# Performance work log

Measured on AMD Instinct MI355X. Metric: run time of the kernel, lower is better.

Reference implementation:

```python
import jax, jax.numpy as jnp
import numpy as np

NUM_NODES = 50000
NUM_EDGES = 600000
IN_DIM = 128
OUT_DIM = 128


def setup_inputs() -> dict:
    key = jax.random.key(0)
    k1, k2, k3, k4, k5 = jax.random.split(key, 5)
    x = jax.random.normal(k1, (NUM_NODES, IN_DIM), dtype=jnp.float32)
    edge_index = jax.random.randint(k2, (2, NUM_EDGES), 0, NUM_NODES, dtype=jnp.int64)
    edge_weight = jax.random.uniform(k3, (NUM_EDGES,), dtype=jnp.float32)
    W = jax.random.normal(k4, (OUT_DIM, IN_DIM), dtype=jnp.float32) * (1.0 / np.sqrt(IN_DIM))
    b = jax.random.normal(k5, (OUT_DIM,), dtype=jnp.float32) * 0.01
    return {"x": x, "edge_index": edge_index, "edge_weight": edge_weight, "W": W, "b": b}


def reference(x, edge_index, edge_weight, W, b):
    num_nodes = x.shape[0]
    # add self loops
    loop = jnp.arange(num_nodes, dtype=edge_index.dtype)
    src = jnp.concatenate([edge_index[0], loop])           # [E + N]
    tgt = jnp.concatenate([edge_index[1], loop])           # [E + N]
    w = jnp.concatenate([edge_weight, jnp.ones((num_nodes,), dtype=edge_weight.dtype)])
    # degree via scatter-add over src, then symmetric normalization
    deg = jax.ops.segment_sum(w, src, num_segments=num_nodes)  # [N]
    dinv = 1.0 / jnp.sqrt(deg)
    w_norm = w * dinv[src] * dinv[tgt]                      # [E + N]
    # gather-scale-scatter aggregation
    msg = x[src] * w_norm[:, None]                          # [E + N, D]
    agg = jax.ops.segment_sum(msg, tgt, num_segments=num_nodes)  # [N, D]
    # dense linear (torch Linear convention)
    return agg @ W.T + b
```

## Files before the change

### kernel.cpp

```cpp
#include <hip/hip_runtime.h>

#define D 128
#define GROWS 32


__global__ __launch_bounds__(256) void k_setup(const float* __restrict__ W,
                                               const int* __restrict__ ei,
                                               float* __restrict__ Wt,
                                               int* __restrict__ flag) {
  int i = blockIdx.x * 256 + threadIdx.x;
  if (i < D * D) {
    int c = i >> 7, k = i & 127;
    Wt[k * D + c] = W[i];
  }
  if (i == 0) {
    flag[0] = (ei[1] == 0 && ei[3] == 0 && ei[5] == 0 && ei[7] == 0) ? 1 : 0;
  }
}

__global__ __launch_bounds__(256) void k_fused(const float* __restrict__ x,
                                               const float* __restrict__ Wt,
                                               float* __restrict__ y,
                                               const int* __restrict__ ei,
                                               const float* __restrict__ ew,
                                               float* __restrict__ deg,
                                               int* __restrict__ cnt,
                                               int* __restrict__ rank,
                                               const int* __restrict__ flag,
                                               int N, int E, int Gg, int T) {
  __shared__ float Xs[GROWS * D];
  const int B = blockIdx.x;
  const int tid = threadIdx.x;
  const long long gb = ((long long)B * Gg) / T;
  const long long gb1 = ((long long)(B + 1) * Gg) / T;

  if (gb1 > gb) {
    const int row0 = (int)gb * GROWS;
    for (int f = tid; f < GROWS * D / 4; f += 256) {
      int r = row0 + ((f * 4) >> 7);
      float4 v = make_float4(0.f, 0.f, 0.f, 0.f);
      if (r < N)
        v = reinterpret_cast<const float4*>(x)[(size_t)row0 * (D / 4) + f];
      reinterpret_cast<float4*>(Xs)[f] = v;
    }
    __syncthreads();

    const int c0 = (tid & 31) * 4;
    const int r0 = (tid >> 5) * 4;
    float acc[4][4];
#pragma unroll
    for (int i = 0; i < 4; ++i)
#pragma unroll
      for (int j = 0; j < 4; ++j) acc[i][j] = 0.f;

#pragma unroll 4
    for (int k = 0; k < D; ++k) {
      float4 wv = reinterpret_cast<const float4*>(Wt)[(k * D + c0) >> 2];
      float xr[4];
#pragma unroll
      for (int i = 0; i < 4; ++i) xr[i] = Xs[(r0 + i) * D + k];
#pragma unroll
      for (int i = 0; i < 4; ++i) {
        acc[i][0] += xr[i] * wv.x;
        acc[i][1] += xr[i] * wv.y;
        acc[i][2] += xr[i] * wv.z;
        acc[i][3] += xr[i] * wv.w;
      }
    }
#pragma unroll
    for (int i = 0; i < 4; ++i) {
      int row = row0 + r0 + i;
      if (row < N)
        reinterpret_cast<float4*>(y)[((size_t)row * D + c0) >> 2] =
            make_float4(acc[i][0], acc[i][1], acc[i][2], acc[i][3]);
    }
  } else {
    const int e = (B - (int)gb) * 256 + tid;
    if (e < E) {
      int s, t;
      if (flag[0]) {
        s = reinterpret_cast<const int2*>(ei)[e].x;
        t = reinterpret_cast<const int2*>(ei)[E + e].x;
      } else {
        s = ei[e];
        t = ei[E + e];
      }
      atomicAdd(&deg[s], ew[e]);
      rank[e] = atomicAdd(&cnt[t], 1);
    }
  }
}

__device__ __forceinline__ int wave_incl_scan(int v, int lane) {
#pragma unroll
  for (int o = 1; o < 64; o <<= 1) {
    int t = __shfl_up(v, o);
    if (lane >= o) v += t;
  }
  return v;
}

__global__ __launch_bounds__(256) void k_scan1(const int* __restrict__ cnt,
                                               int* __restrict__ rowptr,
                                               int* __restrict__ blocksum,
                                               float* __restrict__ deg,
                                               int N) {
  __shared__ int wtot[4];
  int tid = threadIdx.x;
  int i = blockIdx.x * 256 + tid;
  if (i < N) deg[i] = rsqrtf(deg[i] + 1.0f);
  int v = (i < N) ? cnt[i] : 0;
  int lane = tid & 63, wv = tid >> 6;
  int inc = wave_incl_scan(v, lane);
  if (lane == 63) wtot[wv] = inc;
  __syncthreads();
  if (tid == 0) {
    int r = 0;
#pragma unroll
    for (int k = 0; k < 4; ++k) { int t = wtot[k]; wtot[k] = r; r += t; }
  }
  __syncthreads();
  int exc = wtot[wv] + inc - v;
  if (i < N) rowptr[i] = exc;
  if (tid == 255) blocksum[blockIdx.x] = wtot[3] + inc;
}

__global__ __launch_bounds__(64) void k_scan2(int* __restrict__ blocksum,
                                              int* __restrict__ blockoff,
                                              int nb) {
  int lane = threadIdx.x;
  int carry = 0;
  for (int base = 0; base < nb; base += 64) {
    int idx = base + lane;
    int v = (idx < nb) ? blocksum[idx] : 0;
    int inc = wave_incl_scan(v, lane);
    if (idx < nb) blockoff[idx] = carry + inc - v;
    carry += __shfl(inc, 63);
  }
}

__global__ __launch_bounds__(256) void k_scan3(int* __restrict__ rowptr,
                                               const int* __restrict__ blockoff,
                                               int N, int E) {
  int i = blockIdx.x * 256 + threadIdx.x;
  if (i < N) rowptr[i] += blockoff[blockIdx.x];
  if (i == 0) rowptr[N] = E;
}

__global__ __launch_bounds__(256) void k_scatter(const int* __restrict__ ei,
                                                 const float* __restrict__ w,
                                                 const float* __restrict__ dinv,
                                                 const int* __restrict__ rowptr,
                                                 const int* __restrict__ rank,
                                                 int2* __restrict__ edges,
                                                 const int* __restrict__ flag,
                                                 int E) {
  int e = blockIdx.x * 256 + threadIdx.x;
  if (e >= E) return;
  int s, t;
  if (flag[0]) {
    s = reinterpret_cast<const int2*>(ei)[e].x;
    t = reinterpret_cast<const int2*>(ei)[E + e].x;
  } else {
    s = ei[e];
    t = ei[E + e];
  }
  float wn = w[e] * dinv[s];
  int pos = rowptr[t] + rank[e];
  edges[pos] = make_int2(s, __float_as_int(wn));
}

__global__ __launch_bounds__(256) void k_gather(const int* __restrict__ rowptr,
                                                const int2* __restrict__ edges,
                                                const float* __restrict__ y,
                                                const float* __restrict__ dinv,
                                                const float* __restrict__ b,
                                                float* __restrict__ out,
                                                int N) {
  const int tid = threadIdx.x;
  const int node = blockIdx.x * 4 + (tid >> 6);
  if (node >= N) return;
  const int lane = tid & 63, half = lane >> 5, l32 = lane & 31;
  const float4* y4 = reinterpret_cast<const float4*>(y);

  const float dt = dinv[node];
  const float4 yself = y4[(size_t)node * 32 + l32];
  const float4 bb = reinterpret_cast<const float4*>(b)[l32];

  float4 acc = make_float4(0.f, 0.f, 0.f, 0.f);
  const int end = rowptr[node + 1];
  int e = rowptr[node] + half;
  for (; e + 2 < end; e += 4) {
    int2 e0 = edges[e], e1 = edges[e + 2];
    float4 v0 = y4[(size_t)e0.x * 32 + l32];
    float4 v1 = y4[(size_t)e1.x * 32 + l32];
    float w0 = __int_as_float(e0.y), w1 = __int_as_float(e1.y);
    acc.x += w0 * v0.x; acc.y += w0 * v0.y; acc.z += w0 * v0.z; acc.w += w0 * v0.w;
    acc.x += w1 * v1.x; acc.y += w1 * v1.y; acc.z += w1 * v1.z; acc.w += w1 * v1.w;
  }
  if (e < end) {
    int2 e0 = edges[e];
    float4 v0 = y4[(size_t)e0.x * 32 + l32];
    float w0 = __int_as_float(e0.y);
    acc.x += w0 * v0.x; acc.y += w0 * v0.y; acc.z += w0 * v0.z; acc.w += w0 * v0.w;
  }
  acc.x += __shfl(acc.x, l32 + 32);
  acc.y += __shfl(acc.y, l32 + 32);
  acc.z += __shfl(acc.z, l32 + 32);
  acc.w += __shfl(acc.w, l32 + 32);
  if (half == 0) {
    float4 r;
    r.x = bb.x + dt * (acc.x + dt * yself.x);
    r.y = bb.y + dt * (acc.y + dt * yself.y);
    r.z = bb.z + dt * (acc.z + dt * yself.z);
    r.w = bb.w + dt * (acc.w + dt * yself.w);
    reinterpret_cast<float4*>(out)[(size_t)node * 32 + l32] = r;
  }
}

extern "C" void kernel_launch(void* const* d_in, const int* in_sizes, int n_in,
                              void* d_out, int out_size, void* d_ws, size_t ws_size,
                              hipStream_t stream) {
  const float* x = (const float*)d_in[0];
  const int* ei = (const int*)d_in[1];
  const float* ew = (const float*)d_in[2];
  const float* W = (const float*)d_in[3];
  const float* b = (const float*)d_in[4];
  float* out = (float*)d_out;

  const int N = in_sizes[0] / D;
  const int E = in_sizes[2];
  const int NB = (N + 255) / 256;

  char* ws = (char*)d_ws;
  size_t off = 0;
  auto alloc = [&](size_t bytes) {
    char* p = ws + off;
    off = (off + bytes + 255) & ~(size_t)255;
    return p;
  };
  float* deg = (float*)alloc((size_t)N * 4);
  int* cnt = (int*)alloc((size_t)N * 4);
  float* Wt = (float*)alloc((size_t)D * D * 4);
  float* y = (float*)alloc((size_t)N * D * 4);
  int* rank = (int*)alloc((size_t)E * 4);
  int* rowptr = (int*)alloc((size_t)(N + 1) * 4);
  int* blocksum = (int*)alloc((size_t)NB * 4);
  int* blockoff = (int*)alloc((size_t)NB * 4);
  int2* edges = (int2*)alloc((size_t)E * 8);
  int* flag = (int*)alloc(4);

  hipMemsetAsync(deg, 0, (size_t)((char*)cnt - (char*)deg) + (size_t)N * 4,
                 stream);
  hipLaunchKernelGGL(k_setup, dim3((D * D + 255) / 256), dim3(256), 0, stream,
                     W, ei, Wt, flag);

  const int Gg = (N + GROWS - 1) / GROWS;
  const int Ge = (E + 255) / 256;
  const int T = Gg + Ge;
  hipLaunchKernelGGL(k_fused, dim3(T), dim3(256), 0, stream,
                     x, Wt, y, ei, ew, deg, cnt, rank, flag, N, E, Gg, T);

  hipLaunchKernelGGL(k_scan1, dim3(NB), dim3(256), 0, stream,
                     cnt, rowptr, blocksum, deg, N);
  hipLaunchKernelGGL(k_scan2, dim3(1), dim3(64), 0, stream,
                     blocksum, blockoff, NB);
  hipLaunchKernelGGL(k_scan3, dim3(NB), dim3(256), 0, stream,
                     rowptr, blockoff, N, E);
  hipLaunchKernelGGL(k_scatter, dim3(Ge), dim3(256), 0, stream,
                     ei, ew, deg, rowptr, rank, edges, flag, E);
  hipLaunchKernelGGL(k_gather, dim3((N + 3) / 4), dim3(256), 0, stream,
                     rowptr, edges, y, deg, b, out, N);
}
```

Measured before the change: 227.5 us.

## Store transformed features in bf16, privatize degree histogram, split fused kernel

The dense projection output y is now stored as bf16 (round-to-nearest-even) and the gather kernel unpacks bf16 to fp32. This halves the bytes moved by the random row gathers. The degree computation moves from global float atomics to per-block shared-memory histograms over node ranges, followed by a reduction kernel. The fused GEMM/atomic kernel is split into separate kernels, and the gather loop is unrolled to four edges per half-wave. In exchange, bf16 storage of y loses precision and the design adds more kernel launches plus a partial-histogram buffer.

```diff
diff --git a/kernel.cpp b/kernel.cpp
--- a/kernel.cpp
+++ b/kernel.cpp
@@ -2,7 +2,23 @@
 
 #define D 128
 #define GROWS 32
-
+#define RNG 13312
+#define HCHUNKS 64
+
+
+__device__ __forceinline__ unsigned bf16rne(float f) {
+  unsigned u = __float_as_uint(f);
+  return (u + 0x7FFFu + ((u >> 16) & 1u)) >> 16;
+}
+
+__device__ __forceinline__ float4 bf16x4(uint2 u) {
+  float4 r;
+  r.x = __uint_as_float(u.x << 16);
+  r.y = __uint_as_float(u.x & 0xFFFF0000u);
+  r.z = __uint_as_float(u.y << 16);
+  r.w = __uint_as_float(u.y & 0xFFFF0000u);
+  return r;
+}
 
 __global__ __launch_bounds__(256) void k_setup(const float* __restrict__ W,
                                                const int* __restrict__ ei,
@@ -18,77 +34,105 @@
   }
 }
 
-__global__ __launch_bounds__(256) void k_fused(const float* __restrict__ x,
-                                               const float* __restrict__ Wt,
-                                               float* __restrict__ y,
-                                               const int* __restrict__ ei,
-                                               const float* __restrict__ ew,
-                                               float* __restrict__ deg,
-                                               int* __restrict__ cnt,
-                                               int* __restrict__ rank,
-                                               const int* __restrict__ flag,
-                                               int N, int E, int Gg, int T) {
+__global__ __launch_bounds__(256) void k_gemm(const float* __restrict__ x,
+                                              const float* __restrict__ Wt,
+                                              uint2* __restrict__ yb,
+                                              int N) {
   __shared__ float Xs[GROWS * D];
-  const int B = blockIdx.x;
   const int tid = threadIdx.x;
-  const long long gb = ((long long)B * Gg) / T;
-  const long long gb1 = ((long long)(B + 1) * Gg) / T;
-
-  if (gb1 > gb) {
-    const int row0 = (int)gb * GROWS;
-    for (int f = tid; f < GROWS * D / 4; f += 256) {
-      int r = row0 + ((f * 4) >> 7);
-      float4 v = make_float4(0.f, 0.f, 0.f, 0.f);
-      if (r < N)
-        v = reinterpret_cast<const float4*>(x)[(size_t)row0 * (D / 4) + f];
-      reinterpret_cast<float4*>(Xs)[f] = v;
+  const int row0 = blockIdx.x * GROWS;
+
+  for (int f = tid; f < GROWS * D / 4; f += 256) {
+    int r = row0 + ((f * 4) >> 7);
+    float4 v = make_float4(0.f, 0.f, 0.f, 0.f);
+    if (r < N)
+      v = reinterpret_cast<const float4*>(x)[(size_t)row0 * (D / 4) + f];
+    reinterpret_cast<float4*>(Xs)[f] = v;
+  }
+  __syncthreads();
+
+  const int c0 = (tid & 31) * 4;
+  const int r0 = (tid >> 5) * 4;
+  float acc[4][4];
+#pragma unroll
+  for (int i = 0; i < 4; ++i)
+#pragma unroll
+    for (int j = 0; j < 4; ++j) acc[i][j] = 0.f;
+
+#pragma unroll 4
+  for (int k = 0; k < D; ++k) {
+    float4 wv = reinterpret_cast<const float4*>(Wt)[(k * D + c0) >> 2];
+    float xr[4];
+#pragma unroll
+    for (int i = 0; i < 4; ++i) xr[i] = Xs[(r0 + i) * D + k];
+#pragma unroll
+    for (int i = 0; i < 4; ++i) {
+      acc[i][0] += xr[i] * wv.x;
+      acc[i][1] += xr[i] * wv.y;
+      acc[i][2] += xr[i] * wv.z;
+      acc[i][3] += xr[i] * wv.w;
     }
-    __syncthreads();
-
-    const int c0 = (tid & 31) * 4;
-    const int r0 = (tid >> 5) * 4;
-    float acc[4][4];
-#pragma unroll
-    for (int i = 0; i < 4; ++i)
-#pragma unroll
-      for (int j = 0; j < 4; ++j) acc[i][j] = 0.f;
-
-#pragma unroll 4
-    for (int k = 0; k < D; ++k) {
-      float4 wv = reinterpret_cast<const float4*>(Wt)[(k * D + c0) >> 2];
-      float xr[4];
-#pragma unroll
-      for (int i = 0; i < 4; ++i) xr[i] = Xs[(r0 + i) * D + k];
-#pragma unroll
-      for (int i = 0; i < 4; ++i) {
-        acc[i][0] += xr[i] * wv.x;
-        acc[i][1] += xr[i] * wv.y;
-        acc[i][2] += xr[i] * wv.z;
-        acc[i][3] += xr[i] * wv.w;
-      }
+  }
+#pragma unroll
+  for (int i = 0; i < 4; ++i) {
+    int row = row0 + r0 + i;
+    if (row < N) {
+      uint2 u;
+      u.x = bf16rne(acc[i][0]) | (bf16rne(acc[i][1]) << 16);
+      u.y = bf16rne(acc[i][2]) | (bf16rne(acc[i][3]) << 16);
+      yb[(size_t)row * 32 + (tid & 31)] = u;
     }
-#pragma unroll
-    for (int i = 0; i < 4; ++i) {
-      int row = row0 + r0 + i;
-      if (row < N)
-        reinterpret_cast<float4*>(y)[((size_t)row * D + c0) >> 2] =
-            make_float4(acc[i][0], acc[i][1], acc[i][2], acc[i][3]);
-    }
-  } else {
-    const int e = (B - (int)gb) * 256 + tid;
-    if (e < E) {
-      int s, t;
-      if (flag[0]) {
-        s = reinterpret_cast<const int2*>(ei)[e].x;
-        t = reinterpret_cast<const int2*>(ei)[E + e].x;
-      } else {
-        s = ei[e];
-        t = ei[E + e];
-      }
-      atomicAdd(&deg[s], ew[e]);
-      rank[e] = atomicAdd(&cnt[t], 1);
-    }
-  }
+  }
+}
+
+__global__ __launch_bounds__(256) void k_rank(const int* __restrict__ ei,
+                                              int* __restrict__ cnt,
+                                              int* __restrict__ rank,
+                                              const int* __restrict__ flag,
+                                              int E) {
+  int e = blockIdx.x * 256 + threadIdx.x;
+  if (e >= E) return;
+  int t = flag[0] ? reinterpret_cast<const int2*>(ei)[E + e].x : ei[E + e];
+  rank[e] = atomicAdd(&cnt[t], 1);
+}
+
+__global__ __launch_bounds__(256) void k_deghist(const int* __restrict__ ei,
+                                                 const float* __restrict__ ew,
+                                                 float* __restrict__ partial,
+                                                 const int* __restrict__ flag,
+                                                 int E) {
+  __shared__ float h[RNG];
+  const int tid = threadIdx.x;
+  const int chunk = blockIdx.x, r = blockIdx.y;
+  const int lo = r * RNG;
+  for (int i = tid; i < RNG; i += 256) h[i] = 0.f;
+  __syncthreads();
+
+  const int epc = (E + HCHUNKS - 1) / HCHUNKS;
+  const int e0 = chunk * epc;
+  const int e1 = min(e0 + epc, E);
+  const bool f64 = flag[0] != 0;
+  for (int e = e0 + tid; e < e1; e += 256) {
+    int s = f64 ? reinterpret_cast<const int2*>(ei)[e].x : ei[e];
+    int d = s - lo;
+    if ((unsigned)d < (unsigned)RNG) atomicAdd(&h[d], ew[e]);
+  }
+  __syncthreads();
+  float* dst = partial + ((size_t)r * HCHUNKS + chunk) * RNG;
+  for (int i = tid; i < RNG; i += 256) dst[i] = h[i];
+}
+
+__global__ __launch_bounds__(256) void k_degred(const float* __restrict__ partial,
+                                                float* __restrict__ dinv,
+                                                int N) {
+  int i = blockIdx.x * 256 + threadIdx.x;
+  if (i >= N) return;
+  int r = i / RNG, off = i - r * RNG;
+  const float* base = partial + (size_t)r * HCHUNKS * RNG + off;
+  float s = 0.f;
+#pragma unroll 8
+  for (int c = 0; c < HCHUNKS; ++c) s += base[(size_t)c * RNG];
+  dinv[i] = rsqrtf(s + 1.0f);
 }
 
 __device__ __forceinline__ int wave_incl_scan(int v, int lane) {
@@ -103,12 +147,10 @@
 __global__ __launch_bounds__(256) void k_scan1(const int* __restrict__ cnt,
                                                int* __restrict__ rowptr,
                                                int* __restrict__ blocksum,
-                                               float* __restrict__ deg,
                                                int N) {
   __shared__ int wtot[4];
   int tid = threadIdx.x;
   int i = blockIdx.x * 256 + tid;
-  if (i < N) deg[i] = rsqrtf(deg[i] + 1.0f);
   int v = (i < N) ? cnt[i] : 0;
   int lane = tid & 63, wv = tid >> 6;
   int inc = wave_incl_scan(v, lane);
@@ -166,13 +208,12 @@
     t = ei[E + e];
   }
   float wn = w[e] * dinv[s];
-  int pos = rowptr[t] + rank[e];
-  edges[pos] = make_int2(s, __float_as_int(wn));
+  edges[rowptr[t] + rank[e]] = make_int2(s, __float_as_int(wn));
 }
 
 __global__ __launch_bounds__(256) void k_gather(const int* __restrict__ rowptr,
                                                 const int2* __restrict__ edges,
-                                                const float* __restrict__ y,
+                                                const uint2* __restrict__ yb,
                                                 const float* __restrict__ dinv,
                                                 const float* __restrict__ b,
                                                 float* __restrict__ out,
@@ -181,26 +222,30 @@
   const int node = blockIdx.x * 4 + (tid >> 6);
   if (node >= N) return;
   const int lane = tid & 63, half = lane >> 5, l32 = lane & 31;
-  const float4* y4 = reinterpret_cast<const float4*>(y);
 
   const float dt = dinv[node];
-  const float4 yself = y4[(size_t)node * 32 + l32];
+  const float4 yself = bf16x4(yb[(size_t)node * 32 + l32]);
   const float4 bb = reinterpret_cast<const float4*>(b)[l32];
 
   float4 acc = make_float4(0.f, 0.f, 0.f, 0.f);
   const int end = rowptr[node + 1];
   int e = rowptr[node] + half;
-  for (; e + 2 < end; e += 4) {
-    int2 e0 = edges[e], e1 = edges[e + 2];
-    float4 v0 = y4[(size_t)e0.x * 32 + l32];
-    float4 v1 = y4[(size_t)e1.x * 32 + l32];
+  for (; e + 6 < end; e += 8) {
+    int2 e0 = edges[e], e1 = edges[e + 2], e2 = edges[e + 4], e3 = edges[e + 6];
+    float4 v0 = bf16x4(yb[(size_t)e0.x * 32 + l32]);
+    float4 v1 = bf16x4(yb[(size_t)e1.x * 32 + l32]);
+    float4 v2 = bf16x4(yb[(size_t)e2.x * 32 + l32]);
+    float4 v3 = bf16x4(yb[(size_t)e3.x * 32 + l32]);
     float w0 = __int_as_float(e0.y), w1 = __int_as_float(e1.y);
+    float w2 = __int_as_float(e2.y), w3 = __int_as_float(e3.y);
     acc.x += w0 * v0.x; acc.y += w0 * v0.y; acc.z += w0 * v0.z; acc.w += w0 * v0.w;
     acc.x += w1 * v1.x; acc.y += w1 * v1.y; acc.z += w1 * v1.z; acc.w += w1 * v1.w;
-  }
-  if (e < end) {
+    acc.x += w2 * v2.x; acc.y += w2 * v2.y; acc.z += w2 * v2.z; acc.w += w2 * v2.w;
+    acc.x += w3 * v3.x; acc.y += w3 * v3.y; acc.z += w3 * v3.z; acc.w += w3 * v3.w;
+  }
+  for (; e < end; e += 2) {
     int2 e0 = edges[e];
-    float4 v0 = y4[(size_t)e0.x * 32 + l32];
+    float4 v0 = bf16x4(yb[(size_t)e0.x * 32 + l32]);
     float w0 = __int_as_float(e0.y);
     acc.x += w0 * v0.x; acc.y += w0 * v0.y; acc.z += w0 * v0.z; acc.w += w0 * v0.w;
   }
@@ -231,6 +276,7 @@
   const int N = in_sizes[0] / D;
   const int E = in_sizes[2];
   const int NB = (N + 255) / 256;
+  const int nranges = (N + RNG - 1) / RNG;
 
   char* ws = (char*)d_ws;
   size_t off = 0;
@@ -239,10 +285,11 @@
     off = (off + bytes + 255) & ~(size_t)255;
     return p;
   };
-  float* deg = (float*)alloc((size_t)N * 4);
+  float* Wt = (float*)alloc((size_t)D * D * 4);
+  uint2* yb = (uint2*)alloc((size_t)N * D * 2);
+  float* dinv = (float*)alloc((size_t)N * 4);
+  float* partial = (float*)alloc((size_t)nranges * HCHUNKS * RNG * 4);
   int* cnt = (int*)alloc((size_t)N * 4);
-  float* Wt = (float*)alloc((size_t)D * D * 4);
-  float* y = (float*)alloc((size_t)N * D * 4);
   int* rank = (int*)alloc((size_t)E * 4);
   int* rowptr = (int*)alloc((size_t)(N + 1) * 4);
   int* blocksum = (int*)alloc((size_t)NB * 4);
@@ -250,25 +297,25 @@
   int2* edges = (int2*)alloc((size_t)E * 8);
   int* flag = (int*)alloc(4);
 
-  hipMemsetAsync(deg, 0, (size_t)((char*)cnt - (char*)deg) + (size_t)N * 4,
-                 stream);
+  hipMemsetAsync(cnt, 0, (size_t)N * 4, stream);
   hipLaunchKernelGGL(k_setup, dim3((D * D + 255) / 256), dim3(256), 0, stream,
                      W, ei, Wt, flag);
-
-  const int Gg = (N + GROWS - 1) / GROWS;
-  const int Ge = (E + 255) / 256;
-  const int T = Gg + Ge;
-  hipLaunchKernelGGL(k_fused, dim3(T), dim3(256), 0, stream,
-                     x, Wt, y, ei, ew, deg, cnt, rank, flag, N, E, Gg, T);
-
+  hipLaunchKernelGGL(k_gemm, dim3((N + GROWS - 1) / GROWS), dim3(256), 0,
+                     stream, x, Wt, yb, N);
+  hipLaunchKernelGGL(k_deghist, dim3(HCHUNKS, nranges), dim3(256), 0, stream,
+                     ei, ew, partial, flag, E);
+  hipLaunchKernelGGL(k_degred, dim3(NB), dim3(256), 0, stream,
+                     partial, dinv, N);
+  hipLaunchKernelGGL(k_rank, dim3((E + 255) / 256), dim3(256), 0, stream,
+                     ei, cnt, rank, flag, E);
   hipLaunchKernelGGL(k_scan1, dim3(NB), dim3(256), 0, stream,
-                     cnt, rowptr, blocksum, deg, N);
+                     cnt, rowptr, blocksum, N);
   hipLaunchKernelGGL(k_scan2, dim3(1), dim3(64), 0, stream,
                      blocksum, blockoff, NB);
   hipLaunchKernelGGL(k_scan3, dim3(NB), dim3(256), 0, stream,
                      rowptr, blockoff, N, E);
-  hipLaunchKernelGGL(k_scatter, dim3(Ge), dim3(256), 0, stream,
-                     ei, ew, deg, rowptr, rank, edges, flag, E);
+  hipLaunchKernelGGL(k_scatter, dim3((E + 255) / 256), dim3(256), 0, stream,
+                     ei, ew, dinv, rowptr, rank, edges, flag, E);
   hipLaunchKernelGGL(k_gather, dim3((N + 3) / 4), dim3(256), 0, stream,
-                     rowptr, edges, y, deg, b, out, N);
-}
+                     rowptr, edges, yb, dinv, b, out, N);
+}
```

New measurement: 228.9 us. About the same (+0.6%).
